# Kernel optimization log

Hardware: AMD Instinct MI355X
Metric: run time of the kernel (lower is better)

## Reference

```python
import jax, jax.numpy as jnp
import numpy as np

B, T, N, F_DIM = 8, 32, 64, 6
D, H, C = 128, 4, 32          # hidden, spatial heads, head dim
L_SP, L_T, TH = 3, 3, 4       # spatial layers, temporal layers, temporal heads
THD = D // TH                 # temporal head dim
E = N * (N - 1)


def _ln(x, g, b, eps=1e-5):
    mu = x.mean(-1, keepdims=True)
    var = ((x - mu) ** 2).mean(-1, keepdims=True)
    return (x - mu) * jax.lax.rsqrt(var + eps) * g + b


def setup_inputs() -> dict:
    key = jax.random.key(0)
    ks = iter(jax.random.split(key, 64))
    r = lambda *s: jax.random.normal(next(ks), s, jnp.float32) * 0.05
    src_n, dst_n = np.nonzero(~np.eye(N, dtype=bool))
    inp = {
        'input_frames': jax.random.normal(next(ks), (B, T, N, F_DIM), jnp.float32),
        'edge_attr_seq': jax.random.uniform(next(ks), (B, T, E, 1), jnp.float32),
        'proj_W': r(F_DIM, D), 'proj_b': r(D),
        'sp_Wq': r(L_SP, D, D), 'sp_bq': r(L_SP, D),
        'sp_Wk': r(L_SP, D, D), 'sp_bk': r(L_SP, D),
        'sp_Wv': r(L_SP, D, D), 'sp_bv': r(L_SP, D),
        'sp_We': r(L_SP, 1, D), 'sp_be': r(L_SP, D),
        'sp_Ws': r(L_SP, D, D), 'sp_bs': r(L_SP, D),
        'sp_lng': jnp.ones((L_SP, D), jnp.float32), 'sp_lnb': jnp.zeros((L_SP, D), jnp.float32),
        'temporal_pos': r(1, 512, D),
        't_Wqkv': r(L_T, D, 3 * D), 't_bqkv': r(L_T, 3 * D),
        't_Wo': r(L_T, D, D), 't_bo': r(L_T, D),
        't_ln1g': jnp.ones((L_T, D), jnp.float32), 't_ln1b': jnp.zeros((L_T, D), jnp.float32),
        't_W1': r(L_T, D, 4 * D), 't_b1': r(L_T, 4 * D),
        't_W2': r(L_T, 4 * D, D), 't_b2': r(L_T, D),
        't_ln2g': jnp.ones((L_T, D), jnp.float32), 't_ln2b': jnp.zeros((L_T, D), jnp.float32),
        'head_W1': r(D, D), 'head_b1': r(D),
        'head_W2': r(D, F_DIM), 'head_b2': r(F_DIM),
        'edge_index': jnp.asarray(np.stack([src_n, dst_n]), jnp.int32),
    }
    return inp


def _forward(input_frames, edge_attr_seq, proj_W, proj_b, sp_Wq, sp_bq, sp_Wk, sp_bk,
             sp_Wv, sp_bv, sp_We, sp_be, sp_Ws, sp_bs, sp_lng, sp_lnb, temporal_pos,
             t_Wqkv, t_bqkv, t_Wo, t_bo, t_ln1g, t_ln1b, t_W1, t_b1, t_W2, t_b2,
             t_ln2g, t_ln2b, head_W1, head_b1, head_W2, head_b2, edge_index):
    BT = B * T
    Nt = BT * N                                       # total batched nodes
    offs = jnp.arange(BT, dtype=edge_index.dtype) * N
    src = (edge_index[0][None, :] + offs[:, None]).reshape(-1)   # (BT*E,)
    dst = (edge_index[1][None, :] + offs[:, None]).reshape(-1)
    ea = edge_attr_seq.reshape(BT * E, 1)
    h = input_frames.reshape(Nt, F_DIM) @ proj_W + proj_b        # (Nt, D)

    scale = 1.0 / jnp.sqrt(jnp.float32(C))
    for l in range(L_SP):
        q = (h @ sp_Wq[l] + sp_bq[l]).reshape(Nt, H, C)
        k = (h @ sp_Wk[l] + sp_bk[l]).reshape(Nt, H, C)
        v = (h @ sp_Wv[l] + sp_bv[l]).reshape(Nt, H, C)
        e = (ea @ sp_We[l] + sp_be[l]).reshape(-1, H, C)         # (Et, H, C)
        kj = k[src] + e
        alpha = (q[dst] * kj).sum(-1) * scale                    # (Et, H)
        amax = jax.ops.segment_max(alpha, dst, num_segments=Nt)
        ae = jnp.exp(alpha - amax[dst])
        asum = jax.ops.segment_sum(ae, dst, num_segments=Nt)
        w = ae / asum[dst]                                       # segment softmax
        msg = (v[src] + e) * w[..., None]
        agg = jax.ops.segment_sum(msg, dst, num_segments=Nt).reshape(Nt, D)
        out = agg + h @ sp_Ws[l] + sp_bs[l]                      # root/skip term
        h = _ln(h + out, sp_lng[l], sp_lnb[l])

    z = h.reshape(B, T, N, D).transpose(0, 2, 1, 3).reshape(B * N, T, D)
    z = z + temporal_pos[:, :T, :]

    causal = jnp.tril(jnp.ones((T, T), bool))
    tscale = 1.0 / jnp.sqrt(jnp.float32(THD))
    for l in range(L_T):
        qkv = z @ t_Wqkv[l] + t_bqkv[l]
        q, k, v = jnp.split(qkv, 3, axis=-1)
        q = q.reshape(B * N, T, TH, THD)
        k = k.reshape(B * N, T, TH, THD)
        v = v.reshape(B * N, T, TH, THD)
        s = jnp.einsum('bqhd,bkhd->bhqk', q, k) * tscale
        s = jnp.where(causal, s, -jnp.inf)
        a = jax.nn.softmax(s, axis=-1)
        o = jnp.einsum('bhqk,bkhd->bqhd', a, v).reshape(B * N, T, D)
        o = o @ t_Wo[l] + t_bo[l]
        z = _ln(z + o, t_ln1g[l], t_ln1b[l])
        f = jax.nn.gelu(z @ t_W1[l] + t_b1[l], approximate=False) @ t_W2[l] + t_b2[l]
        z = _ln(z + f, t_ln2g[l], t_ln2b[l])

    h_last = z[:, -1, :].reshape(B, N, D)
    pred = jax.nn.gelu(h_last @ head_W1 + head_b1, approximate=False) @ head_W2 + head_b2
    return pred                                                  # (B, N, F)


def reference(input_frames, edge_attr_seq, proj_W, proj_b, sp_Wq, sp_bq, sp_Wk, sp_bk,
              sp_Wv, sp_bv, sp_We, sp_be, sp_Ws, sp_bs, sp_lng, sp_lnb, temporal_pos,
              t_Wqkv, t_bqkv, t_Wo, t_bo, t_ln1g, t_ln1b, t_W1, t_b1, t_W2, t_b2,
              t_ln2g, t_ln2b, head_W1, head_b1, head_W2, head_b2, edge_index):
    return _forward(input_frames, edge_attr_seq, proj_W, proj_b, sp_Wq, sp_bq, sp_Wk,
                    sp_bk, sp_Wv, sp_bv, sp_We, sp_be, sp_Ws, sp_bs, sp_lng, sp_lnb,
                    temporal_pos, t_Wqkv, t_bqkv, t_Wo, t_bo, t_ln1g, t_ln1b, t_W1,
                    t_b1, t_W2, t_b2, t_ln2g, t_ln2b, head_W1, head_b1, head_W2,
                    head_b2, edge_index)
```

## Files before the change

kernel.cpp:

```cpp
#include <hip/hip_runtime.h>
#include <hip/hip_bf16.h>
#include <math.h>

typedef __hip_bfloat16 bf16;
typedef short short8 __attribute__((ext_vector_type(8)));
typedef float floatx4 __attribute__((ext_vector_type(4)));

#define B_    8
#define T_    32
#define N_    64
#define F_    6
#define D_    128
#define E_    4032
#define BT_   256
#define BN_   512

__device__ __forceinline__ float gelu_exact(float x) {
    return 0.5f * x * (1.0f + erff(x * 0.70710678118654752f));
}
__device__ __forceinline__ float bfbits2f(short s) {
    unsigned int u = ((unsigned int)(unsigned short)s) << 16;
    return __uint_as_float(u);
}
__device__ __forceinline__ void ld32lds(const bf16* p, float* o) {
    const short8* sp = (const short8*)p;
#pragma unroll
    for (int i = 0; i < 4; i++) {
        short8 s = sp[i];
#pragma unroll
        for (int j = 0; j < 8; j++) o[i * 8 + j] = bfbits2f(s[j]);
    }
}

struct RepackDesc { const float* W; bf16* out; int K, N, ntt, ntoff, L, start; };
struct RepackArgs { RepackDesc d[9]; int total; };

__global__ void k_repack(RepackArgs ra) {
    int gid = blockIdx.x * blockDim.x + threadIdx.x;
    if (gid >= ra.total) return;
    int fi = 0;
    while (fi < 8 && gid >= ra.d[fi + 1].start) fi++;
    RepackDesc dd = ra.d[fi];
    int r = gid - dd.start;
    int lane = r & 63; r >>= 6;
    int ntiles = dd.N >> 4;
    int nt = r % ntiles; r /= ntiles;
    int ktiles = dd.K >> 5;
    int kt = r % ktiles;
    int l = r / ktiles;
    int quad = lane >> 4, cc = lane & 15;
    const float* Wl = dd.W + (size_t)l * dd.K * dd.N;
    bf16* o = dd.out + ((((size_t)l * ktiles + kt) * dd.ntt + nt + dd.ntoff) * 64 + lane) * 8;
    int kb = kt * 32 + quad * 8;
    int n = nt * 16 + cc;
#pragma unroll
    for (int j = 0; j < 8; j++)
        o[j] = __float2bfloat16(Wl[(size_t)(kb + j) * dd.N + n]);
}

__global__ void k_packbias(const float* __restrict__ bq, const float* __restrict__ bk,
                           const float* __restrict__ bv, float* __restrict__ out) {
    int i = blockIdx.x * blockDim.x + threadIdx.x;
    if (i >= 3 * 384) return;
    int l = i / 384, c = i % 384;
    float v = (c < 128) ? bq[l * 128 + c]
            : (c < 256) ? bk[l * 128 + c - 128]
                        : bv[l * 128 + c - 256];
    out[i] = v;
}

__global__ __launch_bounds__(512, 1)
void k_spatial3(const float* __restrict__ inp, const float* __restrict__ projW,
                const float* __restrict__ projB,
                const short8* __restrict__ BpQKV, const short8* __restrict__ BpWS,
                const float* __restrict__ spb, const float* __restrict__ bs,
                const float* __restrict__ lng, const float* __restrict__ lnb,
                const float* __restrict__ ea, const float* __restrict__ Weg,
                const float* __restrict__ beg, const float* __restrict__ tpos,
                float* __restrict__ z32g) {
    __shared__ short smem[61312];
    bf16* hb = (bf16*)smem;
    bf16* qk = (bf16*)(smem + 8704);
    float* aggf = (float*)(smem + 8704);
    float* fsm = (float*)(smem + 8704);
    bf16* Vt = (bf16*)(smem + 25600);
    bf16* Ps = (bf16*)(smem + 34816);
    float* EAs = (float*)(smem + 53248);

    int bt = blockIdx.x;
    int tid = threadIdx.x;
    int lane = tid & 63, w = tid >> 6;
    int quad = lane >> 4, col = lane & 15;
    int w4 = w & 3, wh = w >> 2;
    const float scale = 0.17677669529663687f;

    for (int i = tid; i < 896; i += 512)
        fsm[i] = (i < 768) ? projW[i] : projB[i - 768];
    {
        const float* eag = ea + (size_t)bt * E_;
        for (int i = tid; i < E_; i += 512) EAs[i] = eag[i];
    }
    __syncthreads();
    float hreg[32];
    if (w < 4) {
#pragma unroll
        for (int r = 0; r < 4; r++) {
            int n = w * 16 + quad * 4 + r;
            const float* xr = inp + (size_t)(bt * 64 + n) * F_;
            float xin[6];
#pragma unroll
            for (int k2 = 0; k2 < 6; k2++) xin[k2] = xr[k2];
#pragma unroll
            for (int tt = 0; tt < 8; tt++) {
                int c = tt * 16 + col;
                float a = fsm[768 + c];
#pragma unroll
                for (int k2 = 0; k2 < 6; k2++) a = fmaf(xin[k2], fsm[k2 * 128 + c], a);
                hreg[tt * 4 + r] = a;
                hb[n * 136 + c] = __float2bfloat16(a);
            }
        }
    }
    __syncthreads();

    for (int l = 0; l < 3; l++) {
        {
            floatx4 acc[12];
#pragma unroll
            for (int tt = 0; tt < 12; tt++) acc[tt] = (floatx4){0.f, 0.f, 0.f, 0.f};
            const short8* bpl = BpQKV + (size_t)l * 6144;
            for (int kt = 0; kt < 4; kt++) {
                short8 a = *(const short8*)&hb[(w4 * 16 + col) * 136 + kt * 32 + quad * 8];
                const short8* bp = bpl + (size_t)(kt * 24 + wh * 12) * 64 + lane;
#pragma unroll
                for (int tt = 0; tt < 12; tt++)
                    acc[tt] = __builtin_amdgcn_mfma_f32_16x16x32_bf16(a, bp[tt * 64], acc[tt], 0, 0, 0);
            }
            const float* bias = spb + l * 384;
#pragma unroll
            for (int tt = 0; tt < 12; tt++) {
                int c = wh * 192 + tt * 16 + col;
                float bv = bias[c];
#pragma unroll
                for (int r = 0; r < 4; r++) {
                    int row = w4 * 16 + quad * 4 + r;
                    bf16 v = __float2bfloat16(acc[tt][r] + bv);
                    if (c < 256) qk[row * 264 + c] = v;
                    else         Vt[(c - 256) * 72 + row] = v;
                }
            }
        }
        __syncthreads();
        int h = w4, half = wh;
        int hoff = h * 32;
        const float* Wel = Weg + l * 128 + hoff;
        const float* bel = beg + l * 128 + hoff;
        float qWe;
        {
            int dst = half * 32 + (lane & 31);
            float qr[32];
            ld32lds(&qk[dst * 264 + hoff], qr);
            float s0 = 0.f, s1 = 0.f, s2 = 0.f, s3 = 0.f;
#pragma unroll
            for (int c2 = 0; c2 < 32; c2 += 4) {
                s0 = fmaf(qr[c2], Wel[c2], s0);
                s1 = fmaf(qr[c2 + 1], Wel[c2 + 1], s1);
                s2 = fmaf(qr[c2 + 2], Wel[c2 + 2], s2);
                s3 = fmaf(qr[c2 + 3], Wel[c2 + 3], s3);
            }
            qWe = (s0 + s1) + (s2 + s3);
        }
        float s[2][4][4], ev[2][4][4];
        {
            short8 aA[2], bB[4];
#pragma unroll
            for (int mtl = 0; mtl < 2; mtl++)
                aA[mtl] = *(const short8*)&qk[((half * 2 + mtl) * 16 + col) * 264 + hoff + quad * 8];
#pragma unroll
            for (int nt = 0; nt < 4; nt++)
                bB[nt] = *(const short8*)&qk[(nt * 16 + col) * 264 + 128 + hoff + quad * 8];
#pragma unroll
            for (int mtl = 0; mtl < 2; mtl++)
#pragma unroll
                for (int nt = 0; nt < 4; nt++) {
                    floatx4 acc = (floatx4){0.f, 0.f, 0.f, 0.f};
                    acc = __builtin_amdgcn_mfma_f32_16x16x32_bf16(aA[mtl], bB[nt], acc, 0, 0, 0);
#pragma unroll
                    for (int r = 0; r < 4; r++) s[mtl][nt][r] = acc[r];
                }
        }
        __syncthreads();
        float ls[2][4], ae[2][4], inv[2][4];
#pragma unroll
        for (int mtl = 0; mtl < 2; mtl++)
#pragma unroll
            for (int r = 0; r < 4; r++) {
                int m = half * 32 + mtl * 16 + quad * 4 + r;
                float qWeR = __shfl(qWe, mtl * 16 + quad * 4 + r, 64);
                float rmax = -1e30f;
#pragma unroll
                for (int nt = 0; nt < 4; nt++) {
                    int n = nt * 16 + col;
                    bool diag = (m == n);
                    int eid = diag ? 0 : (n * 63 + m - (m > n ? 1 : 0));
                    float eav = diag ? 0.f : EAs[eid];
                    ev[mtl][nt][r] = eav;
                    float al = diag ? -1e30f
                                    : scale * (s[mtl][nt][r] + eav * qWeR);
                    s[mtl][nt][r] = al;
                    rmax = fmaxf(rmax, al);
                }
#pragma unroll
                for (int mk2 = 1; mk2 <= 8; mk2 <<= 1)
                    rmax = fmaxf(rmax, __shfl_xor(rmax, mk2, 64));
                float lsum = 0.f, aesum = 0.f;
#pragma unroll
                for (int nt = 0; nt < 4; nt++) {
                    float p = __expf(s[mtl][nt][r] - rmax);
                    s[mtl][nt][r] = p;
                    lsum += p;
                    aesum = fmaf(p, ev[mtl][nt][r], aesum);
                }
#pragma unroll
                for (int mk2 = 1; mk2 <= 8; mk2 <<= 1) {
                    lsum += __shfl_xor(lsum, mk2, 64);
                    aesum += __shfl_xor(aesum, mk2, 64);
                }
                ls[mtl][r] = lsum;
                ae[mtl][r] = aesum;
                inv[mtl][r] = 1.0f / lsum;
            }
        bf16* PsH = Ps + h * 4608;
        floatx4 oacc[2][2];
#pragma unroll
        for (int mtl = 0; mtl < 2; mtl++)
#pragma unroll
            for (int ntB = 0; ntB < 2; ntB++) oacc[mtl][ntB] = (floatx4){0.f, 0.f, 0.f, 0.f};
#pragma unroll
        for (int p = 0; p < 2; p++) {
#pragma unroll
            for (int mtl = 0; mtl < 2; mtl++)
#pragma unroll
                for (int q2 = 0; q2 < 2; q2++) {
                    int nl = q2 * 16 + col;
                    int base0 = (half * 32 + mtl * 16 + quad * 4) * 72 + ((nl >> 3) * 2) * 8 + (nl & 7);
#pragma unroll
                    for (int r = 0; r < 4; r++) {
                        float p_ = s[mtl][2 * p + q2][r];
                        bf16 hi = __float2bfloat16(p_);
                        bf16 lo = __float2bfloat16(p_ - bfbits2f(*(short*)&hi));
                        PsH[base0 + r * 72] = hi;
                        PsH[base0 + r * 72 + 8] = lo;
                    }
                }
            short8 aPh[2], aPl[2], bV[2];
#pragma unroll
            for (int mtl = 0; mtl < 2; mtl++) {
                int rb = (half * 32 + mtl * 16 + col) * 72 + quad * 16;
                aPh[mtl] = *(const short8*)&PsH[rb];
                aPl[mtl] = *(const short8*)&PsH[rb + 8];
            }
#pragma unroll
            for (int ntB = 0; ntB < 2; ntB++)
                bV[ntB] = *(const short8*)&Vt[(hoff + ntB * 16 + col) * 72 + p * 32 + quad * 8];
#pragma unroll
            for (int mtl = 0; mtl < 2; mtl++)
#pragma unroll
                for (int ntB = 0; ntB < 2; ntB++) {
                    oacc[mtl][ntB] = __builtin_amdgcn_mfma_f32_16x16x32_bf16(aPh[mtl], bV[ntB], oacc[mtl][ntB], 0, 0, 0);
                    oacc[mtl][ntB] = __builtin_amdgcn_mfma_f32_16x16x32_bf16(aPl[mtl], bV[ntB], oacc[mtl][ntB], 0, 0, 0);
                }
        }
#pragma unroll
        for (int mtl = 0; mtl < 2; mtl++)
#pragma unroll
            for (int ntB = 0; ntB < 2; ntB++) {
                int c = hoff + ntB * 16 + col;
                float Wc = Wel[ntB * 16 + col];
                float bc = bel[ntB * 16 + col];
#pragma unroll
                for (int r = 0; r < 4; r++) {
                    int m = half * 32 + mtl * 16 + quad * 4 + r;
                    aggf[m * 128 + c] = fmaf(fmaf(ae[mtl][r], Wc, oacc[mtl][ntB][r]),
                                             inv[mtl][r], bc);
                }
            }
        __syncthreads();
        if (w < 4) {
            floatx4 acc2[8];
#pragma unroll
            for (int tt = 0; tt < 8; tt++) acc2[tt] = (floatx4){0.f, 0.f, 0.f, 0.f};
            const short8* bpl = BpWS + (size_t)l * 2048;
            for (int kt = 0; kt < 4; kt++) {
                short8 a = *(const short8*)&hb[(w * 16 + col) * 136 + kt * 32 + quad * 8];
                const short8* bp = bpl + (size_t)(kt * 8) * 64 + lane;
#pragma unroll
                for (int tt = 0; tt < 8; tt++)
                    acc2[tt] = __builtin_amdgcn_mfma_f32_16x16x32_bf16(a, bp[tt * 64], acc2[tt], 0, 0, 0);
            }
            const float* bsl = bs + l * 128;
            float vv[32], rs[4] = {0.f, 0.f, 0.f, 0.f};
#pragma unroll
            for (int tt = 0; tt < 8; tt++) {
                int c = tt * 16 + col;
                float bv = bsl[c];
#pragma unroll
                for (int r = 0; r < 4; r++) {
                    int row = w * 16 + quad * 4 + r;
                    float v = acc2[tt][r] + bv + aggf[row * 128 + c] + hreg[tt * 4 + r];
                    vv[tt * 4 + r] = v;
                    rs[r] += v;
                }
            }
#pragma unroll
            for (int m = 1; m <= 8; m <<= 1)
#pragma unroll
                for (int r = 0; r < 4; r++) rs[r] += __shfl_xor(rs[r], m, 64);
            float mean[4], vs[4] = {0.f, 0.f, 0.f, 0.f};
#pragma unroll
            for (int r = 0; r < 4; r++) mean[r] = rs[r] * (1.0f / 128.0f);
#pragma unroll
            for (int i = 0; i < 32; i++) {
                float d = vv[i] - mean[i & 3];
                vv[i] = d;
                vs[i & 3] += d * d;
            }
#pragma unroll
            for (int m = 1; m <= 8; m <<= 1)
#pragma unroll
                for (int r = 0; r < 4; r++) vs[r] += __shfl_xor(vs[r], m, 64);
            float inv2[4];
#pragma unroll
            for (int r = 0; r < 4; r++) inv2[r] = rsqrtf(vs[r] * (1.0f / 128.0f) + 1e-5f);
            const float* gl = lng + l * 128;
            const float* bl = lnb + l * 128;
            if (l < 2) {
#pragma unroll
                for (int tt = 0; tt < 8; tt++) {
                    int c = tt * 16 + col;
                    float gc = gl[c], bc = bl[c];
#pragma unroll
                    for (int r = 0; r < 4; r++) {
                        float y = vv[tt * 4 + r] * inv2[r] * gc + bc;
                        int n = w * 16 + quad * 4 + r;
                        hreg[tt * 4 + r] = y;
                        hb[n * 136 + c] = __float2bfloat16(y);
                    }
                }
            } else {
                int b = bt >> 5, t_ = bt & 31;
#pragma unroll
                for (int tt = 0; tt < 8; tt++) {
                    int c = tt * 16 + col;
                    float gc = gl[c], bc = bl[c], pc = tpos[t_ * 128 + c];
#pragma unroll
                    for (int r = 0; r < 4; r++) {
                        float y = vv[tt * 4 + r] * inv2[r] * gc + bc;
                        int n = w * 16 + quad * 4 + r;
                        z32g[((size_t)(b * 64 + n) * 32 + t_) * 128 + c] = y + pc;
                    }
                }
            }
        }
        __syncthreads();
    }
}

__global__ __launch_bounds__(512, 4)
void k_temporal3(const float* __restrict__ z32g,
                 const short8* __restrict__ BpQKV, const short8* __restrict__ BpWO,
                 const short8* __restrict__ BpW1, const short8* __restrict__ BpW2,
                 const float* __restrict__ bqkv, const float* __restrict__ bo,
                 const float* __restrict__ ln1g, const float* __restrict__ ln1b,
                 const float* __restrict__ b1, const float* __restrict__ b2,
                 const float* __restrict__ ln2g, const float* __restrict__ ln2b,
                 bf16* __restrict__ zlastb) {
    __shared__ short smem[32000];
    bf16* zb  = (bf16*)smem;
    bf16* qk  = (bf16*)(smem + 4352);
    bf16* Ps  = (bf16*)(smem + 12800);
    bf16* Vt  = (bf16*)(smem + 22016);
    bf16* o16 = (bf16*)(smem + 27136);
    float* lnp = (float*)(smem + 31488);
    bf16* f1  = (bf16*)(smem + 4352);

    int bn = blockIdx.x;
    int tid = threadIdx.x;
    int lane = tid & 63, w = tid >> 6;
    int quad = lane >> 4, col = lane & 15;
    int mt = w & 1, cq = w >> 1;
    const float scale = 0.17677669529663687f;

    for (int i = tid; i < 4096; i += 512) {
        float v = z32g[(size_t)bn * 4096 + i];
        zb[(i >> 7) * 136 + (i & 127)] = __float2bfloat16(v);
    }
    float zreg[8];
#pragma unroll
    for (int t2 = 0; t2 < 2; t2++)
#pragma unroll
        for (int r = 0; r < 4; r++)
            zreg[t2 * 4 + r] = z32g[(size_t)bn * 4096 +
                                    (mt * 16 + quad * 4 + r) * 128 + cq * 32 + t2 * 16 + col];
    __syncthreads();

    for (int l = 0; l < 3; l++) {
        {
            floatx4 acc[6];
#pragma unroll
            for (int tt = 0; tt < 6; tt++) acc[tt] = (floatx4){0.f, 0.f, 0.f, 0.f};
            const short8* bpl = BpQKV + (size_t)l * 6144;
            for (int kt = 0; kt < 4; kt++) {
                short8 a = *(const short8*)&zb[(mt * 16 + col) * 136 + kt * 32 + quad * 8];
                const short8* bp = bpl + (size_t)(kt * 24 + cq * 6) * 64 + lane;
#pragma unroll
                for (int tt = 0; tt < 6; tt++)
                    acc[tt] = __builtin_amdgcn_mfma_f32_16x16x32_bf16(a, bp[tt * 64], acc[tt], 0, 0, 0);
            }
            const float* bias = bqkv + l * 384;
#pragma unroll
            for (int tt = 0; tt < 6; tt++) {
                int c = cq * 96 + tt * 16 + col;
                float bv = bias[c];
#pragma unroll
                for (int r = 0; r < 4; r++) {
                    int row = mt * 16 + quad * 4 + r;
                    bf16 v = __float2bfloat16(acc[tt][r] + bv);
                    if (c < 256) qk[row * 264 + c] = v;
                    else         Vt[(c - 256) * 40 + row] = v;
                }
            }
        }
        __syncthreads();
        {
            int h = w & 3, mh = w >> 2;
            int hoff = h * 32;
            bf16* PsH = Ps + (h * 2 + mh) * 1152;
            float s[2][4];
            short8 aA = *(const short8*)&qk[(mh * 16 + col) * 264 + hoff + quad * 8];
            short8 bB[2];
#pragma unroll
            for (int nt = 0; nt < 2; nt++)
                bB[nt] = *(const short8*)&qk[(nt * 16 + col) * 264 + 128 + hoff + quad * 8];
#pragma unroll
            for (int nt = 0; nt < 2; nt++) {
                floatx4 acc = (floatx4){0.f, 0.f, 0.f, 0.f};
                acc = __builtin_amdgcn_mfma_f32_16x16x32_bf16(aA, bB[nt], acc, 0, 0, 0);
#pragma unroll
                for (int r = 0; r < 4; r++) s[nt][r] = acc[r];
            }
            float inv[4];
#pragma unroll
            for (int r = 0; r < 4; r++) {
                int m = mh * 16 + quad * 4 + r;
                float rmax = -1e30f;
#pragma unroll
                for (int nt = 0; nt < 2; nt++) {
                    int n = nt * 16 + col;
                    float al = (n > m) ? -1e30f : s[nt][r] * scale;
                    s[nt][r] = al;
                    rmax = fmaxf(rmax, al);
                }
#pragma unroll
                for (int mk2 = 1; mk2 <= 8; mk2 <<= 1)
                    rmax = fmaxf(rmax, __shfl_xor(rmax, mk2, 64));
                float lsum = 0.f;
#pragma unroll
                for (int nt = 0; nt < 2; nt++) {
                    float p = __expf(s[nt][r] - rmax);
                    s[nt][r] = p;
                    lsum += p;
                }
#pragma unroll
                for (int mk2 = 1; mk2 <= 8; mk2 <<= 1)
                    lsum += __shfl_xor(lsum, mk2, 64);
                inv[r] = 1.0f / lsum;
            }
#pragma unroll
            for (int nt = 0; nt < 2; nt++) {
                int n = nt * 16 + col;
                int base0 = (quad * 4) * 72 + ((n >> 3) * 2) * 8 + (n & 7);
#pragma unroll
                for (int r = 0; r < 4; r++) {
                    float p_ = s[nt][r];
                    bf16 hi = __float2bfloat16(p_);
                    bf16 lo = __float2bfloat16(p_ - bfbits2f(*(short*)&hi));
                    PsH[base0 + r * 72] = hi;
                    PsH[base0 + r * 72 + 8] = lo;
                }
            }
            floatx4 oacc[2];
#pragma unroll
            for (int nt = 0; nt < 2; nt++) oacc[nt] = (floatx4){0.f, 0.f, 0.f, 0.f};
            short8 aPh = *(const short8*)&PsH[col * 72 + quad * 16];
            short8 aPl = *(const short8*)&PsH[col * 72 + quad * 16 + 8];
            short8 bV[2];
#pragma unroll
            for (int nt = 0; nt < 2; nt++)
                bV[nt] = *(const short8*)&Vt[(hoff + nt * 16 + col) * 40 + quad * 8];
#pragma unroll
            for (int nt = 0; nt < 2; nt++) {
                oacc[nt] = __builtin_amdgcn_mfma_f32_16x16x32_bf16(aPh, bV[nt], oacc[nt], 0, 0, 0);
                oacc[nt] = __builtin_amdgcn_mfma_f32_16x16x32_bf16(aPl, bV[nt], oacc[nt], 0, 0, 0);
            }
#pragma unroll
            for (int nt = 0; nt < 2; nt++) {
                int c = hoff + nt * 16 + col;
#pragma unroll
                for (int r = 0; r < 4; r++)
                    o16[(mh * 16 + quad * 4 + r) * 136 + c] =
                        __float2bfloat16(oacc[nt][r] * inv[r]);
            }
        }
        __syncthreads();
        {
            floatx4 acc2[2];
#pragma unroll
            for (int tt = 0; tt < 2; tt++) acc2[tt] = (floatx4){0.f, 0.f, 0.f, 0.f};
            const short8* bpl = BpWO + (size_t)l * 2048;
            for (int kt = 0; kt < 4; kt++) {
                short8 a = *(const short8*)&o16[(mt * 16 + col) * 136 + kt * 32 + quad * 8];
                const short8* bp = bpl + (size_t)(kt * 8 + cq * 2) * 64 + lane;
#pragma unroll
                for (int tt = 0; tt < 2; tt++)
                    acc2[tt] = __builtin_amdgcn_mfma_f32_16x16x32_bf16(a, bp[tt * 64], acc2[tt], 0, 0, 0);
            }
            const float* bol = bo + l * 128;
            float vv[8], rs[4] = {0.f, 0.f, 0.f, 0.f}, rq[4] = {0.f, 0.f, 0.f, 0.f};
#pragma unroll
            for (int tt = 0; tt < 2; tt++) {
                int c = cq * 32 + tt * 16 + col;
                float bv = bol[c];
#pragma unroll
                for (int r = 0; r < 4; r++) {
                    float v = acc2[tt][r] + bv + zreg[tt * 4 + r];
                    vv[tt * 4 + r] = v;
                    rs[r] += v;
                    rq[r] = fmaf(v, v, rq[r]);
                }
            }
#pragma unroll
            for (int m = 1; m <= 8; m <<= 1)
#pragma unroll
                for (int r = 0; r < 4; r++) {
                    rs[r] += __shfl_xor(rs[r], m, 64);
                    rq[r] += __shfl_xor(rq[r], m, 64);
                }
            if (col == 0) {
#pragma unroll
                for (int r = 0; r < 4; r++) {
                    int row = mt * 16 + quad * 4 + r;
                    lnp[(cq * 32 + row) * 2] = rs[r];
                    lnp[(cq * 32 + row) * 2 + 1] = rq[r];
                }
            }
            __syncthreads();
            const float* gl = ln1g + l * 128;
            const float* bl = ln1b + l * 128;
#pragma unroll
            for (int r = 0; r < 4; r++) {
                int row = mt * 16 + quad * 4 + r;
                float sm = 0.f, sq = 0.f;
#pragma unroll
                for (int q2 = 0; q2 < 4; q2++) {
                    sm += lnp[(q2 * 32 + row) * 2];
                    sq += lnp[(q2 * 32 + row) * 2 + 1];
                }
                float mean = sm * (1.0f / 128.0f);
                float var = sq * (1.0f / 128.0f) - mean * mean;
                float iv = rsqrtf(var + 1e-5f);
#pragma unroll
                for (int tt = 0; tt < 2; tt++) {
                    int c = cq * 32 + tt * 16 + col;
                    float y = (vv[tt * 4 + r] - mean) * iv * gl[c] + bl[c];
                    zreg[tt * 4 + r] = y;
                    zb[row * 136 + c] = __float2bfloat16(y);
                }
            }
        }
        __syncthreads();
        {
            floatx4 acc3[8];
#pragma unroll
            for (int tt = 0; tt < 8; tt++) acc3[tt] = (floatx4){0.f, 0.f, 0.f, 0.f};
            const short8* bpl = BpW1 + (size_t)l * 8192;
            for (int kt = 0; kt < 4; kt++) {
                short8 a = *(const short8*)&zb[(mt * 16 + col) * 136 + kt * 32 + quad * 8];
                const short8* bp = bpl + (size_t)(kt * 32 + cq * 8) * 64 + lane;
#pragma unroll
                for (int tt = 0; tt < 8; tt++)
                    acc3[tt] = __builtin_amdgcn_mfma_f32_16x16x32_bf16(a, bp[tt * 64], acc3[tt], 0, 0, 0);
            }
            const float* b1l = b1 + l * 512;
#pragma unroll
            for (int tt = 0; tt < 8; tt++) {
                int c = cq * 128 + tt * 16 + col;
                float bv = b1l[c];
#pragma unroll
                for (int r = 0; r < 4; r++) {
                    float v = gelu_exact(acc3[tt][r] + bv);
                    f1[(mt * 16 + quad * 4 + r) * 520 + c] = __float2bfloat16(v);
                }
            }
        }
        __syncthreads();
        {
            floatx4 acc4[2];
#pragma unroll
            for (int tt = 0; tt < 2; tt++) acc4[tt] = (floatx4){0.f, 0.f, 0.f, 0.f};
            const short8* bpl = BpW2 + (size_t)l * 8192;
            for (int kt = 0; kt < 16; kt++) {
                short8 a = *(const short8*)&f1[(mt * 16 + col) * 520 + kt * 32 + quad * 8];
                const short8* bp = bpl + (size_t)(kt * 8 + cq * 2) * 64 + lane;
#pragma unroll
                for (int tt = 0; tt < 2; tt++)
                    acc4[tt] = __builtin_amdgcn_mfma_f32_16x16x32_bf16(a, bp[tt * 64], acc4[tt], 0, 0, 0);
            }
            const float* b2l = b2 + l * 128;
            float vv[8], rs[4] = {0.f, 0.f, 0.f, 0.f}, rq[4] = {0.f, 0.f, 0.f, 0.f};
#pragma unroll
            for (int tt = 0; tt < 2; tt++) {
                int c = cq * 32 + tt * 16 + col;
                float bv = b2l[c];
#pragma unroll
                for (int r = 0; r < 4; r++) {
                    float v = acc4[tt][r] + bv + zreg[tt * 4 + r];
                    vv[tt * 4 + r] = v;
                    rs[r] += v;
                    rq[r] = fmaf(v, v, rq[r]);
                }
            }
#pragma unroll
            for (int m = 1; m <= 8; m <<= 1)
#pragma unroll
                for (int r = 0; r < 4; r++) {
                    rs[r] += __shfl_xor(rs[r], m, 64);
                    rq[r] += __shfl_xor(rq[r], m, 64);
                }
            if (col == 0) {
#pragma unroll
                for (int r = 0; r < 4; r++) {
                    int row = mt * 16 + quad * 4 + r;
                    lnp[(cq * 32 + row) * 2] = rs[r];
                    lnp[(cq * 32 + row) * 2 + 1] = rq[r];
                }
            }
            __syncthreads();
            const float* gl = ln2g + l * 128;
            const float* bl = ln2b + l * 128;
#pragma unroll
            for (int r = 0; r < 4; r++) {
                int row = mt * 16 + quad * 4 + r;
                float sm = 0.f, sq = 0.f;
#pragma unroll
                for (int q2 = 0; q2 < 4; q2++) {
                    sm += lnp[(q2 * 32 + row) * 2];
                    sq += lnp[(q2 * 32 + row) * 2 + 1];
                }
                float mean = sm * (1.0f / 128.0f);
                float var = sq * (1.0f / 128.0f) - mean * mean;
                float iv = rsqrtf(var + 1e-5f);
#pragma unroll
                for (int tt = 0; tt < 2; tt++) {
                    int c = cq * 32 + tt * 16 + col;
                    float y = (vv[tt * 4 + r] - mean) * iv * gl[c] + bl[c];
                    zreg[tt * 4 + r] = y;
                    if (l < 2) zb[row * 136 + c] = __float2bfloat16(y);
                    else if (row == 31) zlastb[(size_t)bn * 128 + c] = __float2bfloat16(y);
                }
            }
        }
        __syncthreads();
    }
}

__global__ __launch_bounds__(256)
void k_head(const bf16* __restrict__ zlastb, const short8* __restrict__ BpHW1,
            const float* __restrict__ b1, const float* __restrict__ W2,
            const float* __restrict__ b2, float* __restrict__ out) {
    __shared__ bf16 h1[64 * 136];
    int blk = blockIdx.x;
    int tid = threadIdx.x;
    int lane = tid & 63, w = tid >> 6;
    int quad = lane >> 4, col = lane & 15;
    {
        floatx4 acc[8];
#pragma unroll
        for (int tt = 0; tt < 8; tt++) acc[tt] = (floatx4){0.f, 0.f, 0.f, 0.f};
        const short8* Ap = (const short8*)(zlastb + (size_t)(blk * 64 + w * 16 + col) * 128) + quad;
        for (int kt = 0; kt < 4; kt++) {
            short8 a = Ap[kt * 4];
            const short8* bp = BpHW1 + (size_t)(kt * 8) * 64 + lane;
#pragma unroll
            for (int tt = 0; tt < 8; tt++)
                acc[tt] = __builtin_amdgcn_mfma_f32_16x16x32_bf16(a, bp[tt * 64], acc[tt], 0, 0, 0);
        }
#pragma unroll
        for (int tt = 0; tt < 8; tt++) {
            int c = tt * 16 + col;
            float bv = b1[c];
#pragma unroll
            for (int r = 0; r < 4; r++)
                h1[(w * 16 + quad * 4 + r) * 136 + c] = __float2bfloat16(gelu_exact(acc[tt][r] + bv));
        }
    }
    __syncthreads();
    for (int idx = tid; idx < 512; idx += 256) {
        int row = idx >> 3, c = idx & 7;
        if (c < 6) {
            float a0 = 0.f, a1 = 0.f, a2 = 0.f, a3 = 0.f;
            const bf16* hr = &h1[row * 136];
#pragma unroll 8
            for (int k = 0; k < 128; k += 4) {
                a0 = fmaf(bfbits2f(*(const short*)&hr[k]),     W2[k * 6 + c], a0);
                a1 = fmaf(bfbits2f(*(const short*)&hr[k + 1]), W2[(k + 1) * 6 + c], a1);
                a2 = fmaf(bfbits2f(*(const short*)&hr[k + 2]), W2[(k + 2) * 6 + c], a2);
                a3 = fmaf(bfbits2f(*(const short*)&hr[k + 3]), W2[(k + 3) * 6 + c], a3);
            }
            out[(size_t)(blk * 64 + row) * 6 + c] = (a0 + a1) + (a2 + a3) + b2[c];
        }
    }
}

extern "C" void kernel_launch(void* const* d_in, const int* in_sizes, int n_in,
                              void* d_out, int out_size, void* d_ws, size_t ws_size,
                              hipStream_t stream) {
    const float* input_frames = (const float*)d_in[0];
    const float* edge_attr    = (const float*)d_in[1];
    const float* proj_W  = (const float*)d_in[2];
    const float* proj_b  = (const float*)d_in[3];
    const float* sp_Wq   = (const float*)d_in[4];
    const float* sp_bq   = (const float*)d_in[5];
    const float* sp_Wk   = (const float*)d_in[6];
    const float* sp_bk   = (const float*)d_in[7];
    const float* sp_Wv   = (const float*)d_in[8];
    const float* sp_bv   = (const float*)d_in[9];
    const float* sp_We   = (const float*)d_in[10];
    const float* sp_be   = (const float*)d_in[11];
    const float* sp_Ws   = (const float*)d_in[12];
    const float* sp_bs   = (const float*)d_in[13];
    const float* sp_lng  = (const float*)d_in[14];
    const float* sp_lnb  = (const float*)d_in[15];
    const float* tpos    = (const float*)d_in[16];
    const float* t_Wqkv  = (const float*)d_in[17];
    const float* t_bqkv  = (const float*)d_in[18];
    const float* t_Wo    = (const float*)d_in[19];
    const float* t_bo    = (const float*)d_in[20];
    const float* t_ln1g  = (const float*)d_in[21];
    const float* t_ln1b  = (const float*)d_in[22];
    const float* t_W1    = (const float*)d_in[23];
    const float* t_b1    = (const float*)d_in[24];
    const float* t_W2    = (const float*)d_in[25];
    const float* t_b2    = (const float*)d_in[26];
    const float* t_ln2g  = (const float*)d_in[27];
    const float* t_ln2b  = (const float*)d_in[28];
    const float* head_W1 = (const float*)d_in[29];
    const float* head_b1 = (const float*)d_in[30];
    const float* head_W2 = (const float*)d_in[31];
    const float* head_b2 = (const float*)d_in[32];

    float* f     = (float*)d_ws;
    float* z32g  = f;
    bf16*  zlastb = (bf16*)(f + (1u << 21));
    float* spb   = f + (1u << 21) + 65536;
    bf16* BpBase = (bf16*)(f + (1u << 21) + 65536 + 2048);
    bf16* BpSPQKV = BpBase;
    bf16* BpWS    = BpSPQKV + 147456;
    bf16* BpTQKV  = BpWS + 49152;
    bf16* BpWO    = BpTQKV + 147456;
    bf16* BpW1    = BpWO + 49152;
    bf16* BpW2    = BpW1 + 196608;
    bf16* BpHW1   = BpW2 + 196608;

    RepackArgs ra;
    int s = 0;
    auto mk = [&](int i, const float* W, bf16* out, int K, int N, int ntt, int ntoff, int L) {
        ra.d[i] = {W, out, K, N, ntt, ntoff, L, s};
        s += L * (K >> 5) * (N >> 4) * 64;
    };
    mk(0, sp_Wq, BpSPQKV, 128, 128, 24, 0, 3);
    mk(1, sp_Wk, BpSPQKV, 128, 128, 24, 8, 3);
    mk(2, sp_Wv, BpSPQKV, 128, 128, 24, 16, 3);
    mk(3, sp_Ws, BpWS, 128, 128, 8, 0, 3);
    mk(4, t_Wqkv, BpTQKV, 128, 384, 24, 0, 3);
    mk(5, t_Wo, BpWO, 128, 128, 8, 0, 3);
    mk(6, t_W1, BpW1, 128, 512, 32, 0, 3);
    mk(7, t_W2, BpW2, 512, 128, 8, 0, 3);
    mk(8, head_W1, BpHW1, 128, 128, 8, 0, 1);
    ra.total = s;
    k_repack<<<(s + 255) / 256, 256, 0, stream>>>(ra);
    k_packbias<<<(3 * 384 + 255) / 256, 256, 0, stream>>>(sp_bq, sp_bk, sp_bv, spb);

    k_spatial3<<<BT_, 512, 0, stream>>>(
        input_frames, proj_W, proj_b,
        (const short8*)BpSPQKV, (const short8*)BpWS,
        spb, sp_bs, sp_lng, sp_lnb, edge_attr, sp_We, sp_be, tpos, z32g);

    k_temporal3<<<BN_, 512, 0, stream>>>(
        z32g, (const short8*)BpTQKV, (const short8*)BpWO,
        (const short8*)BpW1, (const short8*)BpW2,
        t_bqkv, t_bo, t_ln1g, t_ln1b, t_b1, t_b2, t_ln2g, t_ln2b, zlastb);

    k_head<<<8, 256, 0, stream>>>(zlastb, (const short8*)BpHW1, head_b1,
                                  head_W2, head_b2, (float*)d_out);
}
```

Measured before the change: 285.3 us.

## Fuse head into temporal kernel, bias packing into repack, prefetch weights, drop barrier

Folds the spatial bias packing into the repack kernel and moves the prediction head into the end of the temporal kernel, removing two launches and the head-weight repack. The spatial kernel's shared buffers are separated so qk, aggregation and edge attributes no longer alias, which lets one barrier go; the aggregation stride is padded to 132. Ws and Wo fragments are prefetched into registers at the start of each layer. In exchange, the head runs as a scalar fp32 loop on 128 threads per block, and the extra registers and larger LDS footprint may limit occupancy.

```diff
diff --git a/kernel.cpp b/kernel.cpp
--- a/kernel.cpp
+++ b/kernel.cpp
@@ -33,13 +33,26 @@
 }
 
 struct RepackDesc { const float* W; bf16* out; int K, N, ntt, ntoff, L, start; };
-struct RepackArgs { RepackDesc d[9]; int total; };
+struct RepackArgs {
+    RepackDesc d[8]; int total;
+    const float *bq, *bk, *bv; float* spb;
+};
 
 __global__ void k_repack(RepackArgs ra) {
     int gid = blockIdx.x * blockDim.x + threadIdx.x;
-    if (gid >= ra.total) return;
+    if (gid >= ra.total) {
+        int i = gid - ra.total;
+        if (i < 3 * 384) {
+            int l = i / 384, c = i % 384;
+            float v = (c < 128) ? ra.bq[l * 128 + c]
+                    : (c < 256) ? ra.bk[l * 128 + c - 128]
+                                : ra.bv[l * 128 + c - 256];
+            ra.spb[i] = v;
+        }
+        return;
+    }
     int fi = 0;
-    while (fi < 8 && gid >= ra.d[fi + 1].start) fi++;
+    while (fi < 7 && gid >= ra.d[fi + 1].start) fi++;
     RepackDesc dd = ra.d[fi];
     int r = gid - dd.start;
     int lane = r & 63; r >>= 6;
@@ -58,17 +71,6 @@
         o[j] = __float2bfloat16(Wl[(size_t)(kb + j) * dd.N + n]);
 }
 
-__global__ void k_packbias(const float* __restrict__ bq, const float* __restrict__ bk,
-                           const float* __restrict__ bv, float* __restrict__ out) {
-    int i = blockIdx.x * blockDim.x + threadIdx.x;
-    if (i >= 3 * 384) return;
-    int l = i / 384, c = i % 384;
-    float v = (c < 128) ? bq[l * 128 + c]
-            : (c < 256) ? bk[l * 128 + c - 128]
-                        : bv[l * 128 + c - 256];
-    out[i] = v;
-}
-
 __global__ __launch_bounds__(512, 1)
 void k_spatial3(const float* __restrict__ inp, const float* __restrict__ projW,
                 const float* __restrict__ projB,
@@ -78,14 +80,14 @@
                 const float* __restrict__ ea, const float* __restrict__ Weg,
                 const float* __restrict__ beg, const float* __restrict__ tpos,
                 float* __restrict__ z32g) {
-    __shared__ short smem[61312];
+    __shared__ short smem[78208];
     bf16* hb = (bf16*)smem;
-    bf16* qk = (bf16*)(smem + 8704);
-    float* aggf = (float*)(smem + 8704);
-    float* fsm = (float*)(smem + 8704);
-    bf16* Vt = (bf16*)(smem + 25600);
-    bf16* Ps = (bf16*)(smem + 34816);
-    float* EAs = (float*)(smem + 53248);
+    bf16* qk = (bf16*)((char*)smem + 17408);
+    bf16* Vt = (bf16*)((char*)smem + 51200);
+    bf16* Ps = (bf16*)((char*)smem + 69632);
+    float* aggf = (float*)((char*)smem + 106496);
+    float* fsm = aggf;
+    float* EAs = (float*)((char*)smem + 140288);
 
     int bt = blockIdx.x;
     int tid = threadIdx.x;
@@ -124,6 +126,15 @@
     __syncthreads();
 
     for (int l = 0; l < 3; l++) {
+        short8 wsF[16];
+        if (w < 4) {
+            const short8* bpl = BpWS + (size_t)l * 2048;
+#pragma unroll
+            for (int kt = 0; kt < 2; kt++)
+#pragma unroll
+                for (int tt = 0; tt < 8; tt++)
+                    wsF[kt * 8 + tt] = bpl[(size_t)(kt * 8 + tt) * 64 + lane];
+        }
         {
             floatx4 acc[12];
 #pragma unroll
@@ -189,7 +200,6 @@
                     for (int r = 0; r < 4; r++) s[mtl][nt][r] = acc[r];
                 }
         }
-        __syncthreads();
         float ls[2][4], ae[2][4], inv[2][4];
 #pragma unroll
         for (int mtl = 0; mtl < 2; mtl++)
@@ -281,7 +291,7 @@
 #pragma unroll
                 for (int r = 0; r < 4; r++) {
                     int m = half * 32 + mtl * 16 + quad * 4 + r;
-                    aggf[m * 128 + c] = fmaf(fmaf(ae[mtl][r], Wc, oacc[mtl][ntB][r]),
+                    aggf[m * 132 + c] = fmaf(fmaf(ae[mtl][r], Wc, oacc[mtl][ntB][r]),
                                              inv[mtl][r], bc);
                 }
             }
@@ -293,10 +303,12 @@
             const short8* bpl = BpWS + (size_t)l * 2048;
             for (int kt = 0; kt < 4; kt++) {
                 short8 a = *(const short8*)&hb[(w * 16 + col) * 136 + kt * 32 + quad * 8];
-                const short8* bp = bpl + (size_t)(kt * 8) * 64 + lane;
-#pragma unroll
-                for (int tt = 0; tt < 8; tt++)
-                    acc2[tt] = __builtin_amdgcn_mfma_f32_16x16x32_bf16(a, bp[tt * 64], acc2[tt], 0, 0, 0);
+#pragma unroll
+                for (int tt = 0; tt < 8; tt++) {
+                    short8 b = (kt < 2) ? wsF[kt * 8 + tt]
+                                        : bpl[(size_t)(kt * 8 + tt) * 64 + lane];
+                    acc2[tt] = __builtin_amdgcn_mfma_f32_16x16x32_bf16(a, b, acc2[tt], 0, 0, 0);
+                }
             }
             const float* bsl = bs + l * 128;
             float vv[32], rs[4] = {0.f, 0.f, 0.f, 0.f};
@@ -307,7 +319,7 @@
 #pragma unroll
                 for (int r = 0; r < 4; r++) {
                     int row = w * 16 + quad * 4 + r;
-                    float v = acc2[tt][r] + bv + aggf[row * 128 + c] + hreg[tt * 4 + r];
+                    float v = acc2[tt][r] + bv + aggf[row * 132 + c] + hreg[tt * 4 + r];
                     vv[tt * 4 + r] = v;
                     rs[r] += v;
                 }
@@ -374,7 +386,9 @@
                  const float* __restrict__ ln1g, const float* __restrict__ ln1b,
                  const float* __restrict__ b1, const float* __restrict__ b2,
                  const float* __restrict__ ln2g, const float* __restrict__ ln2b,
-                 bf16* __restrict__ zlastb) {
+                 const float* __restrict__ hW1, const float* __restrict__ hb1,
+                 const float* __restrict__ hW2, const float* __restrict__ hb2,
+                 float* __restrict__ outp) {
     __shared__ short smem[32000];
     bf16* zb  = (bf16*)smem;
     bf16* qk  = (bf16*)(smem + 4352);
@@ -383,6 +397,7 @@
     bf16* o16 = (bf16*)(smem + 27136);
     float* lnp = (float*)(smem + 31488);
     bf16* f1  = (bf16*)(smem + 4352);
+    float* hz = (float*)(smem + 27136);
 
     int bn = blockIdx.x;
     int tid = threadIdx.x;
@@ -404,7 +419,17 @@
                                     (mt * 16 + quad * 4 + r) * 128 + cq * 32 + t2 * 16 + col];
     __syncthreads();
 
+    float yout[2];
     for (int l = 0; l < 3; l++) {
+        short8 woF[8];
+        {
+            const short8* bpl = BpWO + (size_t)l * 2048;
+#pragma unroll
+            for (int kt = 0; kt < 4; kt++)
+#pragma unroll
+                for (int tt = 0; tt < 2; tt++)
+                    woF[kt * 2 + tt] = bpl[(size_t)(kt * 8 + cq * 2 + tt) * 64 + lane];
+        }
         {
             floatx4 acc[6];
 #pragma unroll
@@ -517,13 +542,11 @@
             floatx4 acc2[2];
 #pragma unroll
             for (int tt = 0; tt < 2; tt++) acc2[tt] = (floatx4){0.f, 0.f, 0.f, 0.f};
-            const short8* bpl = BpWO + (size_t)l * 2048;
             for (int kt = 0; kt < 4; kt++) {
                 short8 a = *(const short8*)&o16[(mt * 16 + col) * 136 + kt * 32 + quad * 8];
-                const short8* bp = bpl + (size_t)(kt * 8 + cq * 2) * 64 + lane;
 #pragma unroll
                 for (int tt = 0; tt < 2; tt++)
-                    acc2[tt] = __builtin_amdgcn_mfma_f32_16x16x32_bf16(a, bp[tt * 64], acc2[tt], 0, 0, 0);
+                    acc2[tt] = __builtin_amdgcn_mfma_f32_16x16x32_bf16(a, woF[kt * 2 + tt], acc2[tt], 0, 0, 0);
             }
             const float* bol = bo + l * 128;
             float vv[8], rs[4] = {0.f, 0.f, 0.f, 0.f}, rq[4] = {0.f, 0.f, 0.f, 0.f};
@@ -666,59 +689,29 @@
                     float y = (vv[tt * 4 + r] - mean) * iv * gl[c] + bl[c];
                     zreg[tt * 4 + r] = y;
                     if (l < 2) zb[row * 136 + c] = __float2bfloat16(y);
-                    else if (row == 31) zlastb[(size_t)bn * 128 + c] = __float2bfloat16(y);
+                    else if (row == 31) yout[tt] = y;
                 }
             }
         }
         __syncthreads();
     }
-}
-
-__global__ __launch_bounds__(256)
-void k_head(const bf16* __restrict__ zlastb, const short8* __restrict__ BpHW1,
-            const float* __restrict__ b1, const float* __restrict__ W2,
-            const float* __restrict__ b2, float* __restrict__ out) {
-    __shared__ bf16 h1[64 * 136];
-    int blk = blockIdx.x;
-    int tid = threadIdx.x;
-    int lane = tid & 63, w = tid >> 6;
-    int quad = lane >> 4, col = lane & 15;
-    {
-        floatx4 acc[8];
-#pragma unroll
-        for (int tt = 0; tt < 8; tt++) acc[tt] = (floatx4){0.f, 0.f, 0.f, 0.f};
-        const short8* Ap = (const short8*)(zlastb + (size_t)(blk * 64 + w * 16 + col) * 128) + quad;
-        for (int kt = 0; kt < 4; kt++) {
-            short8 a = Ap[kt * 4];
-            const short8* bp = BpHW1 + (size_t)(kt * 8) * 64 + lane;
-#pragma unroll
-            for (int tt = 0; tt < 8; tt++)
-                acc[tt] = __builtin_amdgcn_mfma_f32_16x16x32_bf16(a, bp[tt * 64], acc[tt], 0, 0, 0);
-        }
-#pragma unroll
-        for (int tt = 0; tt < 8; tt++) {
-            int c = tt * 16 + col;
-            float bv = b1[c];
-#pragma unroll
-            for (int r = 0; r < 4; r++)
-                h1[(w * 16 + quad * 4 + r) * 136 + c] = __float2bfloat16(gelu_exact(acc[tt][r] + bv));
-        }
+    if (mt == 1 && quad == 3) {
+        hz[cq * 32 + col] = yout[0];
+        hz[cq * 32 + 16 + col] = yout[1];
     }
     __syncthreads();
-    for (int idx = tid; idx < 512; idx += 256) {
-        int row = idx >> 3, c = idx & 7;
-        if (c < 6) {
-            float a0 = 0.f, a1 = 0.f, a2 = 0.f, a3 = 0.f;
-            const bf16* hr = &h1[row * 136];
-#pragma unroll 8
-            for (int k = 0; k < 128; k += 4) {
-                a0 = fmaf(bfbits2f(*(const short*)&hr[k]),     W2[k * 6 + c], a0);
-                a1 = fmaf(bfbits2f(*(const short*)&hr[k + 1]), W2[(k + 1) * 6 + c], a1);
-                a2 = fmaf(bfbits2f(*(const short*)&hr[k + 2]), W2[(k + 2) * 6 + c], a2);
-                a3 = fmaf(bfbits2f(*(const short*)&hr[k + 3]), W2[(k + 3) * 6 + c], a3);
-            }
-            out[(size_t)(blk * 64 + row) * 6 + c] = (a0 + a1) + (a2 + a3) + b2[c];
-        }
+    if (tid < 128) {
+        float acc = hb1[tid];
+        for (int k = 0; k < 128; k++)
+            acc = fmaf(hz[k], hW1[k * 128 + tid], acc);
+        hz[128 + tid] = gelu_exact(acc);
+    }
+    __syncthreads();
+    if (tid < 6) {
+        float o = hb2[tid];
+        for (int k = 0; k < 128; k++)
+            o = fmaf(hz[128 + k], hW2[k * 6 + tid], o);
+        outp[(size_t)bn * 6 + tid] = o;
     }
 }
 
@@ -761,16 +754,14 @@
 
     float* f     = (float*)d_ws;
     float* z32g  = f;
-    bf16*  zlastb = (bf16*)(f + (1u << 21));
-    float* spb   = f + (1u << 21) + 65536;
-    bf16* BpBase = (bf16*)(f + (1u << 21) + 65536 + 2048);
+    float* spb   = f + (1u << 21);
+    bf16* BpBase = (bf16*)(f + (1u << 21) + 2048);
     bf16* BpSPQKV = BpBase;
     bf16* BpWS    = BpSPQKV + 147456;
     bf16* BpTQKV  = BpWS + 49152;
     bf16* BpWO    = BpTQKV + 147456;
     bf16* BpW1    = BpWO + 49152;
     bf16* BpW2    = BpW1 + 196608;
-    bf16* BpHW1   = BpW2 + 196608;
 
     RepackArgs ra;
     int s = 0;
@@ -786,10 +777,9 @@
     mk(5, t_Wo, BpWO, 128, 128, 8, 0, 3);
     mk(6, t_W1, BpW1, 128, 512, 32, 0, 3);
     mk(7, t_W2, BpW2, 512, 128, 8, 0, 3);
-    mk(8, head_W1, BpHW1, 128, 128, 8, 0, 1);
     ra.total = s;
-    k_repack<<<(s + 255) / 256, 256, 0, stream>>>(ra);
-    k_packbias<<<(3 * 384 + 255) / 256, 256, 0, stream>>>(sp_bq, sp_bk, sp_bv, spb);
+    ra.bq = sp_bq; ra.bk = sp_bk; ra.bv = sp_bv; ra.spb = spb;
+    k_repack<<<(s + 1152 + 255) / 256, 256, 0, stream>>>(ra);
 
     k_spatial3<<<BT_, 512, 0, stream>>>(
         input_frames, proj_W, proj_b,
@@ -799,8 +789,6 @@
     k_temporal3<<<BN_, 512, 0, stream>>>(
         z32g, (const short8*)BpTQKV, (const short8*)BpWO,
         (const short8*)BpW1, (const short8*)BpW2,
-        t_bqkv, t_bo, t_ln1g, t_ln1b, t_b1, t_b2, t_ln2g, t_ln2b, zlastb);
-
-    k_head<<<8, 256, 0, stream>>>(zlastb, (const short8*)BpHW1, head_b1,
-                                  head_W2, head_b2, (float*)d_out);
+        t_bqkv, t_bo, t_ln1g, t_ln1b, t_b1, t_b2, t_ln2g, t_ln2b,
+        head_W1, head_b1, head_W2, head_b2, (float*)d_out);
 }
```

New measurement: 339.4 us. 1.19x slower.
